# Kernel optimization log

Hardware: AMD Instinct MI355X
Metric: run time of the kernel (lower is better)

Reference implementation:

```python
import jax, jax.numpy as jnp
import numpy as np

DIM = 768
HEADS = 12
HIDDEN = 3072  # int(dim * mlp_ratio)
DEGREE = 3
EPS = 1e-5


def layer_norm(x, g, b):
    m = jnp.mean(x, axis=-1, keepdims=True)
    v = jnp.mean((x - m) ** 2, axis=-1, keepdims=True)
    return (x - m) * jax.lax.rsqrt(v + EPS) * g + b


def cheby_layer(x, coeffs):
    # x: (B, N, I); coeffs: (I, O, DEGREE+1)
    t = jnp.tanh(x)
    theta = jnp.arccos(t)  # (B, N, I)
    d = jnp.arange(DEGREE + 1, dtype=x.dtype)
    basis = jnp.cos(theta[..., None] * d)  # (B, N, I, D)
    return jnp.einsum('bnid,iod->bno', basis, coeffs)


def setup_inputs() -> dict:
    key = jax.random.key(0)
    ks = jax.random.split(key, 9)
    B, N, C, H = 32, 197, DIM, HIDDEN
    x = jax.random.normal(ks[0], (B, N, C), dtype=jnp.float32)
    g1 = jnp.ones((C,), jnp.float32)
    b1 = jnp.zeros((C,), jnp.float32)
    w_qkv = jax.random.normal(ks[1], (C, 3 * C), jnp.float32) * (C ** -0.5)
    w_proj = jax.random.normal(ks[2], (C, C), jnp.float32) * (C ** -0.5)
    b_proj = jnp.zeros((C,), jnp.float32)
    g2 = jnp.ones((C,), jnp.float32)
    b2 = jnp.zeros((C,), jnp.float32)
    c1 = jax.random.normal(ks[3], (C, H, DEGREE + 1), jnp.float32) / (C * (DEGREE + 1))
    c2 = jax.random.normal(ks[4], (H, C, DEGREE + 1), jnp.float32) / (H * (DEGREE + 1))
    return {"x": x, "g1": g1, "b1": b1, "w_qkv": w_qkv, "w_proj": w_proj,
            "b_proj": b_proj, "g2": g2, "b2": b2, "c1": c1, "c2": c2}


def reference(x, g1, b1, w_qkv, w_proj, b_proj, g2, b2, c1, c2):
    B, N, C = x.shape
    hd = C // HEADS
    scale = hd ** -0.5
    # --- attention branch ---
    h = layer_norm(x, g1, b1)
    qkv = (h @ w_qkv).reshape(B, N, 3, HEADS, hd).transpose(2, 0, 3, 1, 4)
    q, k, v = qkv[0], qkv[1], qkv[2]  # (B, H, N, hd)
    attn = jax.nn.softmax(jnp.einsum('bhnd,bhmd->bhnm', q, k) * scale, axis=-1)
    o = jnp.einsum('bhnm,bhmd->bhnd', attn, v).transpose(0, 2, 1, 3).reshape(B, N, C)
    x = x + o @ w_proj + b_proj
    # --- ChebyKAN MLP branch ---
    h = layer_norm(x, g2, b2)
    h = cheby_layer(h, c1)   # (B, N, HIDDEN)
    h = cheby_layer(h, c2)   # (B, N, C)
    return x + h
```

## Files before the change

### kernel.cpp

```cpp
#include <hip/hip_runtime.h>
#include <hip/hip_bf16.h>
#include <cmath>
#include <cstdint>
#include <cstddef>

#define DEV __device__ __forceinline__

typedef __attribute__((ext_vector_type(4))) float f32x4;
typedef __attribute__((ext_vector_type(8))) short bf16x8;
typedef __attribute__((ext_vector_type(4))) unsigned int u32x4;
typedef __attribute__((ext_vector_type(4))) unsigned short u16x4;

constexpr int NBATCH = 32;
constexpr int SEQ    = 197;
constexpr int CH     = 768;
constexpr int H3     = 3 * CH;
constexpr int NHEADS = 12;
constexpr int HD     = 64;
constexpr int HID    = 3072;
constexpr int TOK    = NBATCH * SEQ;
constexpr int TOKP   = 6400;
constexpr float LNEPS = 1e-5f;

DEV unsigned short f2bf(float f) {
  unsigned int u = __builtin_bit_cast(unsigned int, f);
  u += 0x7fffu + ((u >> 16) & 1u);
  return (unsigned short)(u >> 16);
}
DEV float bf2f(unsigned short s) {
  unsigned int u = ((unsigned int)s) << 16;
  return __builtin_bit_cast(float, u);
}

DEV float fast_tanh(float x) {
  const float e = __expf(2.f * x);
  return 1.f - 2.f * __builtin_amdgcn_rcpf(e + 1.f);
}

DEV void async_copy16(void* lds, const void* gmem) {
  __builtin_amdgcn_global_load_lds(
      (const __attribute__((address_space(1))) unsigned int*)gmem,
      (__attribute__((address_space(3))) unsigned int*)lds, 16, 0, 0);
}

template <int DO_TANH>
__global__ void ln_kernel(const float* __restrict__ xin, const float* __restrict__ gg,
                          const float* __restrict__ bb, unsigned short* __restrict__ outp) {
  const int row  = blockIdx.x * 4 + (threadIdx.x >> 6);
  const int lane = threadIdx.x & 63;
  if (row >= TOK) {
    u16x4 z = {0, 0, 0, 0};
    #pragma unroll
    for (int c = 0; c < 3; ++c)
      *(u16x4*)&outp[(size_t)row * CH + c * 256 + lane * 4] = z;
    return;
  }
  f32x4 v[3];
  float s = 0.f, s2 = 0.f;
  #pragma unroll
  for (int c = 0; c < 3; ++c) {
    v[c] = *(const f32x4*)&xin[(size_t)row * CH + c * 256 + lane * 4];
    #pragma unroll
    for (int e = 0; e < 4; ++e) { s += v[c][e]; s2 += v[c][e] * v[c][e]; }
  }
  #pragma unroll
  for (int off = 32; off; off >>= 1) { s += __shfl_xor(s, off); s2 += __shfl_xor(s2, off); }
  const float mean = s * (1.f / CH);
  const float var  = s2 * (1.f / CH) - mean * mean;
  const float rs   = rsqrtf(var + LNEPS);
  #pragma unroll
  for (int c = 0; c < 3; ++c) {
    f32x4 gv = *(const f32x4*)&gg[c * 256 + lane * 4];
    f32x4 bv = *(const f32x4*)&bb[c * 256 + lane * 4];
    u16x4 o;
    #pragma unroll
    for (int e = 0; e < 4; ++e) {
      float f = (v[c][e] - mean) * rs * gv[e] + bv[e];
      if (DO_TANH) f = fast_tanh(f);
      o[e] = f2bf(f);
    }
    *(u16x4*)&outp[(size_t)row * CH + c * 256 + lane * 4] = o;
  }
}

__global__ void transpose_bf16(const float* __restrict__ in, unsigned short* __restrict__ outp,
                               int K, int N) {
  __shared__ unsigned short tile[64][65];
  const int k0 = blockIdx.x * 64, n0 = blockIdx.y * 64;
  const int tc = threadIdx.x & 63, tr = threadIdx.x >> 6;
  #pragma unroll
  for (int rr = 0; rr < 64; rr += 4)
    tile[rr + tr][tc] = f2bf(in[(size_t)(k0 + rr + tr) * N + n0 + tc]);
  __syncthreads();
  #pragma unroll
  for (int rr = 0; rr < 64; rr += 4)
    outp[(size_t)(n0 + rr + tr) * K + k0 + tc] = tile[tc][rr + tr];
}

__global__ void cheb_combine(const float* __restrict__ cc, unsigned short* __restrict__ outp,
                             float* __restrict__ partial, int I, int O) {
  __shared__ unsigned short t1[64][65];
  __shared__ unsigned short t2[64][65];
  __shared__ unsigned short t3[64][65];
  __shared__ float psum[4][64];
  const int i0 = blockIdx.x * 64, o0 = blockIdx.y * 64;
  const int tc = threadIdx.x & 63, tr = threadIdx.x >> 6;
  float bs = 0.f;
  #pragma unroll
  for (int rr = 0; rr < 64; rr += 4) {
    f32x4 v = *(const f32x4*)&cc[((size_t)(i0 + rr + tr) * O + (o0 + tc)) * 4];
    t1[rr + tr][tc] = f2bf(v[1] - 3.f * v[3]);
    t2[rr + tr][tc] = f2bf(2.f * v[2]);
    t3[rr + tr][tc] = f2bf(4.f * v[3]);
    bs += v[0] - v[2];
  }
  psum[tr][tc] = bs;
  __syncthreads();
  const size_t plane = (size_t)O * I;
  #pragma unroll
  for (int rr = 0; rr < 64; rr += 4) {
    size_t ob = (size_t)(o0 + rr + tr) * I + i0 + tc;
    outp[ob]             = t1[tc][rr + tr];
    outp[ob + plane]     = t2[tc][rr + tr];
    outp[ob + 2 * plane] = t3[tc][rr + tr];
  }
  if (tr == 0)
    partial[(size_t)blockIdx.x * O + o0 + tc] =
        psum[0][tc] + psum[1][tc] + psum[2][tc] + psum[3][tc];
}

__global__ void bias_finish(const float* __restrict__ partial, float* __restrict__ bias,
                            int nblk, int O) {
  const int o = blockIdx.x * 256 + threadIdx.x;
  float s = 0.f;
  for (int k = 0; k < nblk; ++k) s += partial[(size_t)k * O + o];
  bias[o] = s;
}

__global__ void zero_pad_rows(unsigned short* __restrict__ p) {
  const size_t idx = ((size_t)blockIdx.x * 256 + threadIdx.x) * 4;
  u16x4 z = {0, 0, 0, 0};
  *(u16x4*)&p[(size_t)TOK * CH + idx] = z;
}

template <int EPI>
__global__ __launch_bounds__(256)
void gemm_kernel(const unsigned short* __restrict__ A,
                 const unsigned short* __restrict__ BT,
                 const int Ktot, const int Nn,
                 const float* __restrict__ bias,
                 const float* __restrict__ resid,
                 void* __restrict__ Cout) {
  __shared__ __align__(16) unsigned short As[2][128 * 32];
  __shared__ __align__(16) unsigned short Bs[2][128 * 32];
  const int t = threadIdx.x;
  const int lane = t & 63;
  const int wid = t >> 6;
  const int wm = wid >> 1, wn = wid & 1;
  const int bm = blockIdx.x * 128;
  const int bn = blockIdx.y * 128;
  const int srow = t >> 2;
  const int scol = (t & 3) * 8;
  const int nkt = Ktot >> 5;
  f32x4 acc[4][4] = {};

  auto stage = [&](int buf, int kt) {
    const int kk = kt << 5;
    char* lb = (char*)&Bs[buf][0] + (wid << 10);
    async_copy16(lb,        &BT[(size_t)(bn + srow) * Ktot + kk + scol]);
    async_copy16(lb + 4096, &BT[(size_t)(bn + 64 + srow) * Ktot + kk + scol]);
    char* la = (char*)&As[buf][0] + (wid << 10);
    async_copy16(la,        &A[(size_t)(bm + srow) * Ktot + kk + scol]);
    async_copy16(la + 4096, &A[(size_t)(bm + 64 + srow) * Ktot + kk + scol]);
  };

  int cur = 0;
  stage(0, 0);
  for (int kt = 0; kt < nkt; ++kt) {
    if (kt + 1 < nkt) {
      stage(cur ^ 1, kt + 1);
      asm volatile("s_waitcnt vmcnt(4)" ::: "memory");
    } else {
      asm volatile("s_waitcnt vmcnt(0)" ::: "memory");
    }
    __builtin_amdgcn_s_barrier();
    __builtin_amdgcn_sched_barrier(0);
    bf16x8 af[4], bfr[4];
    const int frow = lane & 15;
    const int fk = (lane >> 4) * 8;
    #pragma unroll
    for (int m = 0; m < 4; ++m)
      af[m] = *(const bf16x8*)&As[cur][(wm * 64 + m * 16 + frow) * 32 + fk];
    #pragma unroll
    for (int n = 0; n < 4; ++n)
      bfr[n] = *(const bf16x8*)&Bs[cur][(wn * 64 + n * 16 + frow) * 32 + fk];
    #pragma unroll
    for (int m = 0; m < 4; ++m)
      #pragma unroll
      for (int n = 0; n < 4; ++n)
        acc[m][n] = __builtin_amdgcn_mfma_f32_16x16x32_bf16(af[m], bfr[n], acc[m][n], 0, 0, 0);
    __builtin_amdgcn_s_barrier();
    cur ^= 1;
  }
  #pragma unroll
  for (int m = 0; m < 4; ++m) {
    #pragma unroll
    for (int n = 0; n < 4; ++n) {
      #pragma unroll
      for (int r = 0; r < 4; ++r) {
        const int row = bm + wm * 64 + m * 16 + (lane >> 4) * 4 + r;
        const int col = bn + wn * 64 + n * 16 + (lane & 15);
        const float v = acc[m][n][r];
        if (EPI == 0) {
          ((unsigned short*)Cout)[(size_t)row * Nn + col] = f2bf(v);
        } else {
          float o = 0.f;
          if (row < TOK) o = v + bias[col] + resid[(size_t)row * Nn + col];
          ((float*)Cout)[(size_t)row * Nn + col] = o;
        }
      }
    }
  }
}

template <int EPI>
__global__ __launch_bounds__(256, 4)
void cheb_gemm(const unsigned short* __restrict__ A,
               const unsigned short* __restrict__ BT,
               const int Ktot, const int Nn,
               const float* __restrict__ bias,
               const float* __restrict__ resid,
               void* __restrict__ Cout) {
  __shared__ __align__(16) unsigned short As[2][128 * 32];
  __shared__ __align__(16) unsigned short Bs[2][3 * 64 * 32];
  const int t = threadIdx.x, lane = t & 63, wid = t >> 6;
  const int bm = blockIdx.x * 128, bn = blockIdx.y * 64;
  const int srow = t >> 2, scol = (t & 3) * 8;
  const int nkt = Ktot >> 5;
  f32x4 acc[2][4] = {};

  auto stage = [&](int buf, int kt) {
    const int kk = kt << 5;
    char* la = (char*)&As[buf][0] + (wid << 10);
    async_copy16(la,        &A[(size_t)(bm + srow) * Ktot + kk + scol]);
    async_copy16(la + 4096, &A[(size_t)(bm + 64 + srow) * Ktot + kk + scol]);
    char* lb = (char*)&Bs[buf][0] + (wid << 10);
    #pragma unroll
    for (int p = 0; p < 3; ++p)
      async_copy16(lb + p * 4096, &BT[((size_t)p * Nn + bn + srow) * Ktot + kk + scol]);
  };

  int cur = 0;
  stage(0, 0);
  for (int kt = 0; kt < nkt; ++kt) {
    if (kt + 1 < nkt) {
      stage(cur ^ 1, kt + 1);
      asm volatile("s_waitcnt vmcnt(5)" ::: "memory");
    } else {
      asm volatile("s_waitcnt vmcnt(0)" ::: "memory");
    }
    __builtin_amdgcn_s_barrier();
    __builtin_amdgcn_sched_barrier(0);
    const int frow = lane & 15, fk = (lane >> 4) * 8;
    bf16x8 a1[2], a2[2], a3[2];
    #pragma unroll
    for (int m = 0; m < 2; ++m)
      a1[m] = *(const bf16x8*)&As[cur][(wid * 32 + m * 16 + frow) * 32 + fk];
    #pragma unroll
    for (int m = 0; m < 2; ++m) {
      const unsigned int* w = (const unsigned int*)&a1[m];
      unsigned int sq[4], cu[4];
      #pragma unroll
      for (int j = 0; j < 4; ++j) {
        const unsigned int u = w[j];
        const float lo = __builtin_bit_cast(float, u << 16);
        const float hi = __builtin_bit_cast(float, u & 0xffff0000u);
        const float lo2 = lo * lo, hi2 = hi * hi;
        const float lo3 = lo2 * lo, hi3 = hi2 * hi;
        sq[j] = (__builtin_bit_cast(unsigned int, hi2) & 0xffff0000u) |
                (__builtin_bit_cast(unsigned int, lo2) >> 16);
        cu[j] = (__builtin_bit_cast(unsigned int, hi3) & 0xffff0000u) |
                (__builtin_bit_cast(unsigned int, lo3) >> 16);
      }
      a2[m] = *(const bf16x8*)sq;
      a3[m] = *(const bf16x8*)cu;
    }
    #pragma unroll
    for (int p = 0; p < 3; ++p) {
      bf16x8 br[4];
      #pragma unroll
      for (int n = 0; n < 4; ++n)
        br[n] = *(const bf16x8*)&Bs[cur][(p * 64 + n * 16 + frow) * 32 + fk];
      #pragma unroll
      for (int m = 0; m < 2; ++m) {
        const bf16x8 a = (p == 0) ? a1[m] : (p == 1) ? a2[m] : a3[m];
        #pragma unroll
        for (int n = 0; n < 4; ++n)
          acc[m][n] = __builtin_amdgcn_mfma_f32_16x16x32_bf16(a, br[n], acc[m][n], 0, 0, 0);
      }
    }
    __builtin_amdgcn_s_barrier();
    cur ^= 1;
  }
  #pragma unroll
  for (int m = 0; m < 2; ++m) {
    #pragma unroll
    for (int n = 0; n < 4; ++n) {
      #pragma unroll
      for (int r = 0; r < 4; ++r) {
        const int row = bm + wid * 32 + m * 16 + (lane >> 4) * 4 + r;
        const int col = bn + n * 16 + (lane & 15);
        const float v = acc[m][n][r];
        if (EPI == 0) {
          ((unsigned short*)Cout)[(size_t)row * Nn + col] = f2bf(fast_tanh(v + bias[col]));
        } else {
          if (row < TOK)
            ((float*)Cout)[(size_t)row * Nn + col] = v + bias[col] + resid[(size_t)row * Nn + col];
        }
      }
    }
  }
}

__global__ __launch_bounds__(256)
void attn_kernel(const unsigned short* __restrict__ qkv, unsigned short* __restrict__ aout) {
  constexpr int VSTR = 232;
  __shared__ __align__(16) unsigned short Vlds[64 * VSTR];
  __shared__ __align__(16) unsigned short Plds[4][16 * VSTR];
  const int bh = blockIdx.x;
  const int b = bh / NHEADS, hh = bh - b * NHEADS;
  const int t = threadIdx.x, lane = t & 63, wid = t >> 6;
  const size_t base = (size_t)b * SEQ * H3;
  const int part = t & 7, key0 = t >> 3;
  for (int it = 0; it < 7; ++it) {
    const int key = key0 + it * 32;
    u32x4 raw = {0, 0, 0, 0};
    if (key < SEQ)
      raw = *(const u32x4*)&qkv[base + (size_t)key * H3 + 2 * CH + hh * HD + part * 8];
    const unsigned short* us = (const unsigned short*)&raw;
    #pragma unroll
    for (int e = 0; e < 8; ++e)
      Vlds[(part * 8 + e) * VSTR + key] = us[e];
  }
  for (int idx = t; idx < 4 * 16 * 16; idx += 256) {
    const int buf = idx >> 8, rr = (idx >> 4) & 15, ccc = idx & 15;
    Plds[buf][rr * VSTR + 208 + ccc] = 0;
  }
  __syncthreads();

  for (int qt = wid; qt < 13; qt += 4) {
    const int qrow = qt * 16 + (lane & 15);
    const size_t qbase = base + (size_t)qrow * H3 + hh * HD + (lane >> 4) * 8;
    const bf16x8 qf0 = *(const bf16x8*)&qkv[qbase];
    const bf16x8 qf1 = *(const bf16x8*)&qkv[qbase + 32];
    float sv[13][4];
    #pragma unroll
    for (int ktile = 0; ktile < 13; ++ktile) {
      const int keyc = ktile * 16 + (lane & 15);
      const size_t kbase = base + (size_t)keyc * H3 + CH + hh * HD + (lane >> 4) * 8;
      const bf16x8 kf0 = *(const bf16x8*)&qkv[kbase];
      const bf16x8 kf1 = *(const bf16x8*)&qkv[kbase + 32];
      f32x4 s = {0.f, 0.f, 0.f, 0.f};
      s = __builtin_amdgcn_mfma_f32_16x16x32_bf16(qf0, kf0, s, 0, 0, 0);
      s = __builtin_amdgcn_mfma_f32_16x16x32_bf16(qf1, kf1, s, 0, 0, 0);
      const bool valid = keyc < SEQ;
      #pragma unroll
      for (int r = 0; r < 4; ++r)
        sv[ktile][r] = valid ? s[r] * 0.125f : -INFINITY;
    }
    float rsum[4];
    #pragma unroll
    for (int r = 0; r < 4; ++r) {
      float mx = -INFINITY;
      #pragma unroll
      for (int kt2 = 0; kt2 < 13; ++kt2) mx = fmaxf(mx, sv[kt2][r]);
      #pragma unroll
      for (int off = 1; off < 16; off <<= 1) mx = fmaxf(mx, __shfl_xor(mx, off));
      float sum = 0.f;
      #pragma unroll
      for (int kt2 = 0; kt2 < 13; ++kt2) {
        const float p = __expf(sv[kt2][r] - mx);
        sv[kt2][r] = p;
        sum += p;
      }
      #pragma unroll
      for (int off = 1; off < 16; off <<= 1) sum += __shfl_xor(sum, off);
      rsum[r] = sum;
    }
    const int g4 = (lane >> 4) * 4;
    #pragma unroll
    for (int kt2 = 0; kt2 < 13; ++kt2)
      #pragma unroll
      for (int r = 0; r < 4; ++r)
        Plds[wid][(g4 + r) * VSTR + kt2 * 16 + (lane & 15)] = f2bf(sv[kt2][r]);
    asm volatile("s_waitcnt lgkmcnt(0)" ::: "memory");
    f32x4 oacc[4] = {};
    #pragma unroll
    for (int ks = 0; ks < 7; ++ks) {
      const bf16x8 pf = *(const bf16x8*)&Plds[wid][(lane & 15) * VSTR + ks * 32 + (lane >> 4) * 8];
      #pragma unroll
      for (int n = 0; n < 4; ++n) {
        const bf16x8 vf = *(const bf16x8*)&Vlds[(n * 16 + (lane & 15)) * VSTR + ks * 32 + (lane >> 4) * 8];
        oacc[n] = __builtin_amdgcn_mfma_f32_16x16x32_bf16(pf, vf, oacc[n], 0, 0, 0);
      }
    }
    #pragma unroll
    for (int n = 0; n < 4; ++n)
      #pragma unroll
      for (int r = 0; r < 4; ++r) {
        const int q = qt * 16 + g4 + r;
        if (q < SEQ) {
          const float val = oacc[n][r] / rsum[r];
          aout[(size_t)(b * SEQ + q) * CH + hh * HD + n * 16 + (lane & 15)] = f2bf(val);
        }
      }
  }
}

extern "C" void kernel_launch(void* const* d_in, const int* in_sizes, int n_in,
                              void* d_out, int out_size, void* d_ws, size_t ws_size,
                              hipStream_t stream) {
  const float* x      = (const float*)d_in[0];
  const float* g1     = (const float*)d_in[1];
  const float* b1     = (const float*)d_in[2];
  const float* w_qkv  = (const float*)d_in[3];
  const float* w_proj = (const float*)d_in[4];
  const float* b_proj = (const float*)d_in[5];
  const float* g2     = (const float*)d_in[6];
  const float* b2     = (const float*)d_in[7];
  const float* c1     = (const float*)d_in[8];
  const float* c2     = (const float*)d_in[9];

  char* ws = (char*)d_ws;
  size_t off = 0;
  auto alloc = [&](size_t bytes) { size_t o = off; off += (bytes + 255) & ~(size_t)255; return o; };
  unsigned short* h      = (unsigned short*)(ws + alloc((size_t)TOKP * CH * 2));
  unsigned short* wqkvT  = (unsigned short*)(ws + alloc((size_t)H3 * CH * 2));
  unsigned short* wprojT = (unsigned short*)(ws + alloc((size_t)CH * CH * 2));
  unsigned short* c1T    = (unsigned short*)(ws + alloc((size_t)3 * HID * CH * 2));
  unsigned short* c2T    = (unsigned short*)(ws + alloc((size_t)3 * CH * HID * 2));
  float* bias1           = (float*)(ws + alloc((size_t)HID * 4));
  float* bias2           = (float*)(ws + alloc((size_t)CH * 4));
  float* part1           = (float*)(ws + alloc((size_t)(CH / 64) * HID * 4));
  float* part2           = (float*)(ws + alloc((size_t)(HID / 64) * CH * 4));
  unsigned short* qkvb   = (unsigned short*)(ws + alloc((size_t)TOKP * H3 * 2));
  unsigned short* aoutb  = (unsigned short*)(ws + alloc((size_t)TOKP * CH * 2));
  float* xmid            = (float*)(ws + alloc((size_t)TOKP * CH * 4));
  unsigned short* tb     = (unsigned short*)(ws + alloc((size_t)TOKP * CH * 2));
  unsigned short* ub     = (unsigned short*)(ws + alloc((size_t)TOKP * HID * 2));
  (void)ws_size; (void)in_sizes; (void)n_in; (void)out_size;

  transpose_bf16<<<dim3(CH / 64, H3 / 64), 256, 0, stream>>>(w_qkv, wqkvT, CH, H3);
  transpose_bf16<<<dim3(CH / 64, CH / 64), 256, 0, stream>>>(w_proj, wprojT, CH, CH);
  cheb_combine<<<dim3(CH / 64, HID / 64), 256, 0, stream>>>(c1, c1T, part1, CH, HID);
  cheb_combine<<<dim3(HID / 64, CH / 64), 256, 0, stream>>>(c2, c2T, part2, HID, CH);
  bias_finish<<<dim3(HID / 256), 256, 0, stream>>>(part1, bias1, CH / 64, HID);
  bias_finish<<<dim3(CH / 256), 256, 0, stream>>>(part2, bias2, HID / 64, CH);
  zero_pad_rows<<<dim3(72), 256, 0, stream>>>(aoutb);

  ln_kernel<0><<<dim3(TOKP / 4), 256, 0, stream>>>(x, g1, b1, h);
  gemm_kernel<0><<<dim3(TOKP / 128, H3 / 128), 256, 0, stream>>>(h, wqkvT, CH, H3,
                                                                 nullptr, nullptr, qkvb);
  attn_kernel<<<dim3(NBATCH * NHEADS), 256, 0, stream>>>(qkvb, aoutb);
  gemm_kernel<1><<<dim3(TOKP / 128, CH / 128), 256, 0, stream>>>(aoutb, wprojT, CH, CH,
                                                                 b_proj, x, xmid);
  ln_kernel<1><<<dim3(TOKP / 4), 256, 0, stream>>>(xmid, g2, b2, tb);
  cheb_gemm<0><<<dim3(TOKP / 128, HID / 64), 256, 0, stream>>>(tb, c1T, CH, HID,
                                                               bias1, nullptr, ub);
  cheb_gemm<1><<<dim3(TOKP / 128, CH / 64), 256, 0, stream>>>(ub, c2T, HID, CH,
                                                              bias2, xmid, (float*)d_out);
}
```

Before: 412.0 us.

## Swizzle LDS layout, split-K second Cheby GEMM, load A directly to registers

```diff
diff --git a/kernel.cpp b/kernel.cpp
--- a/kernel.cpp
+++ b/kernel.cpp
@@ -20,6 +20,7 @@
 constexpr int HID    = 3072;
 constexpr int TOK    = NBATCH * SEQ;
 constexpr int TOKP   = 6400;
+constexpr int KSPLIT = 2;
 constexpr float LNEPS = 1e-5f;
 
 DEV unsigned short f2bf(float f) {
@@ -160,18 +161,19 @@
   const int bm = blockIdx.x * 128;
   const int bn = blockIdx.y * 128;
   const int srow = t >> 2;
-  const int scol = (t & 3) * 8;
+  const int ssw  = ((t & 3) ^ ((t >> 2) & 3) ^ ((t >> 4) & 3)) * 8;
+  const int rslot = ((lane >> 4) ^ (lane & 3) ^ ((lane >> 2) & 3)) * 8;
   const int nkt = Ktot >> 5;
   f32x4 acc[4][4] = {};
 
   auto stage = [&](int buf, int kt) {
     const int kk = kt << 5;
     char* lb = (char*)&Bs[buf][0] + (wid << 10);
-    async_copy16(lb,        &BT[(size_t)(bn + srow) * Ktot + kk + scol]);
-    async_copy16(lb + 4096, &BT[(size_t)(bn + 64 + srow) * Ktot + kk + scol]);
+    async_copy16(lb,        &BT[(size_t)(bn + srow) * Ktot + kk + ssw]);
+    async_copy16(lb + 4096, &BT[(size_t)(bn + 64 + srow) * Ktot + kk + ssw]);
     char* la = (char*)&As[buf][0] + (wid << 10);
-    async_copy16(la,        &A[(size_t)(bm + srow) * Ktot + kk + scol]);
-    async_copy16(la + 4096, &A[(size_t)(bm + 64 + srow) * Ktot + kk + scol]);
+    async_copy16(la,        &A[(size_t)(bm + srow) * Ktot + kk + ssw]);
+    async_copy16(la + 4096, &A[(size_t)(bm + 64 + srow) * Ktot + kk + ssw]);
   };
 
   int cur = 0;
@@ -187,13 +189,12 @@
     __builtin_amdgcn_sched_barrier(0);
     bf16x8 af[4], bfr[4];
     const int frow = lane & 15;
-    const int fk = (lane >> 4) * 8;
     #pragma unroll
     for (int m = 0; m < 4; ++m)
-      af[m] = *(const bf16x8*)&As[cur][(wm * 64 + m * 16 + frow) * 32 + fk];
+      af[m] = *(const bf16x8*)&As[cur][(wm * 64 + m * 16 + frow) * 32 + rslot];
     #pragma unroll
     for (int n = 0; n < 4; ++n)
-      bfr[n] = *(const bf16x8*)&Bs[cur][(wn * 64 + n * 16 + frow) * 32 + fk];
+      bfr[n] = *(const bf16x8*)&Bs[cur][(wn * 64 + n * 16 + frow) * 32 + rslot];
     #pragma unroll
     for (int m = 0; m < 4; ++m)
       #pragma unroll
@@ -227,48 +228,55 @@
 __global__ __launch_bounds__(256, 4)
 void cheb_gemm(const unsigned short* __restrict__ A,
                const unsigned short* __restrict__ BT,
-               const int Ktot, const int Nn,
+               const int Ktot, const int Nn, const int kchunk,
                const float* __restrict__ bias,
-               const float* __restrict__ resid,
                void* __restrict__ Cout) {
-  __shared__ __align__(16) unsigned short As[2][128 * 32];
-  __shared__ __align__(16) unsigned short Bs[2][3 * 64 * 32];
+  __shared__ __align__(16) unsigned short Bs[3][3 * 64 * 32];
   const int t = threadIdx.x, lane = t & 63, wid = t >> 6;
   const int bm = blockIdx.x * 128, bn = blockIdx.y * 64;
-  const int srow = t >> 2, scol = (t & 3) * 8;
-  const int nkt = Ktot >> 5;
+  const int kbase = (int)blockIdx.z * kchunk;
+  const int nkt = kchunk >> 5;
+  const int srow = t >> 2;
+  const int ssw  = ((t & 3) ^ ((t >> 2) & 3) ^ ((t >> 4) & 3)) * 8;
+  const int frow = lane & 15;
+  const int rslot = ((lane >> 4) ^ (lane & 3) ^ ((lane >> 2) & 3)) * 8;
+  const int arow = bm + wid * 32 + frow;
+  const int ak   = (lane >> 4) * 8;
+  const size_t pstride = (size_t)Nn * Ktot;
   f32x4 acc[2][4] = {};
 
-  auto stage = [&](int buf, int kt) {
-    const int kk = kt << 5;
-    char* la = (char*)&As[buf][0] + (wid << 10);
-    async_copy16(la,        &A[(size_t)(bm + srow) * Ktot + kk + scol]);
-    async_copy16(la + 4096, &A[(size_t)(bm + 64 + srow) * Ktot + kk + scol]);
+  auto stageB = [&](int buf, int kt) {
+    const int kk = kbase + (kt << 5);
     char* lb = (char*)&Bs[buf][0] + (wid << 10);
     #pragma unroll
     for (int p = 0; p < 3; ++p)
-      async_copy16(lb + p * 4096, &BT[((size_t)p * Nn + bn + srow) * Ktot + kk + scol]);
+      async_copy16(lb + p * 4096,
+                   &BT[(size_t)p * pstride + (size_t)(bn + srow) * Ktot + kk + ssw]);
   };
-
-  int cur = 0;
-  stage(0, 0);
-  for (int kt = 0; kt < nkt; ++kt) {
-    if (kt + 1 < nkt) {
-      stage(cur ^ 1, kt + 1);
-      asm volatile("s_waitcnt vmcnt(5)" ::: "memory");
-    } else {
-      asm volatile("s_waitcnt vmcnt(0)" ::: "memory");
-    }
+  auto loadA = [&](bf16x8 (&dst)[2], int kt) {
+    const int kk = kbase + (kt << 5) + ak;
+    #pragma unroll
+    for (int m = 0; m < 2; ++m)
+      dst[m] = *(const bf16x8*)&A[(size_t)(arow + m * 16) * Ktot + kk];
+  };
+
+  bf16x8 aA[2], aB[2];
+  stageB(0, 0);
+  loadA(aA, 0);
+  if (nkt > 1) stageB(1, 1);
+
+  auto body = [&](bf16x8 (&curA)[2], bf16x8 (&nxtA)[2], int kt) {
+    if (kt + 1 < nkt) asm volatile("s_waitcnt vmcnt(3)" ::: "memory");
+    else              asm volatile("s_waitcnt vmcnt(0)" ::: "memory");
     __builtin_amdgcn_s_barrier();
     __builtin_amdgcn_sched_barrier(0);
-    const int frow = lane & 15, fk = (lane >> 4) * 8;
-    bf16x8 a1[2], a2[2], a3[2];
-    #pragma unroll
-    for (int m = 0; m < 2; ++m)
-      a1[m] = *(const bf16x8*)&As[cur][(wid * 32 + m * 16 + frow) * 32 + fk];
+    const unsigned short* bp = &Bs[kt % 3][0];
+    if (kt + 1 < nkt) loadA(nxtA, kt + 1);
+    if (kt + 2 < nkt) stageB((kt + 2) % 3, kt + 2);
+    bf16x8 a2[2], a3[2];
     #pragma unroll
     for (int m = 0; m < 2; ++m) {
-      const unsigned int* w = (const unsigned int*)&a1[m];
+      const unsigned int* w = (const unsigned int*)&curA[m];
       unsigned int sq[4], cu[4];
       #pragma unroll
       for (int j = 0; j < 4; ++j) {
@@ -290,18 +298,22 @@
       bf16x8 br[4];
       #pragma unroll
       for (int n = 0; n < 4; ++n)
-        br[n] = *(const bf16x8*)&Bs[cur][(p * 64 + n * 16 + frow) * 32 + fk];
+        br[n] = *(const bf16x8*)&bp[(p * 64 + n * 16 + frow) * 32 + rslot];
       #pragma unroll
       for (int m = 0; m < 2; ++m) {
-        const bf16x8 a = (p == 0) ? a1[m] : (p == 1) ? a2[m] : a3[m];
+        const bf16x8 a = (p == 0) ? curA[m] : (p == 1) ? a2[m] : a3[m];
         #pragma unroll
         for (int n = 0; n < 4; ++n)
           acc[m][n] = __builtin_amdgcn_mfma_f32_16x16x32_bf16(a, br[n], acc[m][n], 0, 0, 0);
       }
     }
-    __builtin_amdgcn_s_barrier();
-    cur ^= 1;
-  }
+  };
+
+  for (int kt = 0; kt < nkt; kt += 2) {
+    body(aA, aB, kt);
+    body(aB, aA, kt + 1);
+  }
+
   #pragma unroll
   for (int m = 0; m < 2; ++m) {
     #pragma unroll
@@ -314,12 +326,30 @@
         if (EPI == 0) {
           ((unsigned short*)Cout)[(size_t)row * Nn + col] = f2bf(fast_tanh(v + bias[col]));
         } else {
-          if (row < TOK)
-            ((float*)Cout)[(size_t)row * Nn + col] = v + bias[col] + resid[(size_t)row * Nn + col];
+          ((float*)Cout)[((size_t)blockIdx.z * TOKP + row) * Nn + col] = v;
         }
       }
     }
   }
+}
+
+__global__ void cheb2_reduce(const float* __restrict__ part, const float* __restrict__ bias,
+                             const float* __restrict__ resid, float* __restrict__ outp) {
+  const size_t idx = ((size_t)blockIdx.x * 256 + threadIdx.x) * 4;
+  const int col = (int)(idx % CH);
+  f32x4 s = *(const f32x4*)&part[idx];
+  #pragma unroll
+  for (int z = 1; z < KSPLIT; ++z) {
+    f32x4 p = *(const f32x4*)&part[(size_t)z * TOKP * CH + idx];
+    #pragma unroll
+    for (int e = 0; e < 4; ++e) s[e] += p[e];
+  }
+  const f32x4 bv = *(const f32x4*)&bias[col];
+  const f32x4 rv = *(const f32x4*)&resid[idx];
+  f32x4 o;
+  #pragma unroll
+  for (int e = 0; e < 4; ++e) o[e] = s[e] + bv[e] + rv[e];
+  *(f32x4*)&outp[idx] = o;
 }
 
 __global__ __launch_bounds__(256)
@@ -448,6 +478,7 @@
   float* xmid            = (float*)(ws + alloc((size_t)TOKP * CH * 4));
   unsigned short* tb     = (unsigned short*)(ws + alloc((size_t)TOKP * CH * 2));
   unsigned short* ub     = (unsigned short*)(ws + alloc((size_t)TOKP * HID * 2));
+  float* partK           = (float*)(ws + alloc((size_t)KSPLIT * TOKP * CH * 4));
   (void)ws_size; (void)in_sizes; (void)n_in; (void)out_size;
 
   transpose_bf16<<<dim3(CH / 64, H3 / 64), 256, 0, stream>>>(w_qkv, wqkvT, CH, H3);
@@ -465,8 +496,10 @@
   gemm_kernel<1><<<dim3(TOKP / 128, CH / 128), 256, 0, stream>>>(aoutb, wprojT, CH, CH,
                                                                  b_proj, x, xmid);
   ln_kernel<1><<<dim3(TOKP / 4), 256, 0, stream>>>(xmid, g2, b2, tb);
-  cheb_gemm<0><<<dim3(TOKP / 128, HID / 64), 256, 0, stream>>>(tb, c1T, CH, HID,
-                                                               bias1, nullptr, ub);
-  cheb_gemm<1><<<dim3(TOKP / 128, CH / 64), 256, 0, stream>>>(ub, c2T, HID, CH,
-                                                              bias2, xmid, (float*)d_out);
-}
+  cheb_gemm<0><<<dim3(TOKP / 128, HID / 64, 1), 256, 0, stream>>>(tb, c1T, CH, HID, CH,
+                                                                  bias1, ub);
+  cheb_gemm<1><<<dim3(TOKP / 128, CH / 64, KSPLIT), 256, 0, stream>>>(ub, c2T, HID, CH,
+                                                                      HID / KSPLIT,
+                                                                      nullptr, partK);
+  cheb2_reduce<<<dim3(TOK * CH / 1024), 256, 0, stream>>>(partK, bias2, xmid, (float*)d_out);
+}
```

Measured after the change: 425.6 us. 1.03x slower.
